# Optimization experiments

Measured on AMD Instinct MI355X. Metric: run time of the kernel, lower is better.

## Reference

```python
import jax, jax.numpy as jnp
import numpy as np

B, S, C = 128, 512, 128


def setup_inputs() -> dict:
    key = jax.random.key(0)
    k1, k2, k3, k4, k5 = jax.random.split(key, 5)
    emissions = jax.random.normal(k1, (B, S, C), dtype=jnp.float32)
    tags = jax.random.randint(k2, (B, S), 0, C, dtype=jnp.int64)
    mask = jnp.ones((B, S), dtype=bool)  # mask[:,0] must be True
    transitions = jax.random.normal(k3, (C, C), dtype=jnp.float32)
    start_transitions = jax.random.normal(k4, (C,), dtype=jnp.float32)
    end_transitions = jax.random.normal(k5, (C,), dtype=jnp.float32)
    return {"emissions": emissions, "tags": tags, "mask": mask,
            "transitions": transitions, "start_transitions": start_transitions,
            "end_transitions": end_transitions}


def _gold_score(emissions, tags, mask, transitions, start_t, end_t):
    # score of the gold tag path, fully vectorized over time
    b = jnp.arange(emissions.shape[0])
    score = start_t[tags[:, 0]] + emissions[b, 0, tags[:, 0]]            # [B]
    emit_t = jnp.take_along_axis(emissions, tags[..., None], axis=2)[..., 0]  # [B,S]
    trans_t = transitions[tags[:, :-1], tags[:, 1:]]                     # [B,S-1]
    score = score + jnp.sum((emit_t[:, 1:] + trans_t) * mask[:, 1:].astype(emissions.dtype), axis=1)
    last_idx = jnp.sum(mask.astype(jnp.int32), axis=1) - 1               # [B]
    last_tags = jnp.take_along_axis(tags, last_idx[:, None], axis=1)[:, 0]
    return score + end_t[last_tags]


def _partition(emissions, mask, transitions, start_t, end_t):
    # forward algorithm: sequential logsumexp recurrence via lax.scan
    alpha0 = start_t[None, :] + emissions[:, 0]                          # [B,C]

    def step(alpha, inp):
        emit_t, mask_t = inp                                             # [B,C], [B]
        score = alpha[:, :, None] + transitions[None] + emit_t[:, None, :]  # [B,C,C]
        new_alpha = jax.nn.logsumexp(score, axis=1)                      # [B,C]
        alpha = jnp.where(mask_t[:, None], new_alpha, alpha)
        return alpha, None

    xs = (jnp.moveaxis(emissions[:, 1:], 1, 0), mask[:, 1:].T)           # [S-1,B,C], [S-1,B]
    alpha, _ = jax.lax.scan(step, alpha0, xs)
    return jax.nn.logsumexp(alpha + end_t[None, :], axis=1)              # [B]


def reference(emissions, tags, mask, transitions, start_transitions, end_transitions):
    gold = _gold_score(emissions, tags, mask, transitions, start_transitions, end_transitions)
    part = _partition(emissions, mask, transitions, start_transitions, end_transitions)
    return -(gold - part).mean()
```

## Files before the change

kernel.cpp:

```cpp
#include <hip/hip_runtime.h>

#define BB 128
#define SS 512
#define CC 128

__device__ __forceinline__ void barrier_lgkm() {
    asm volatile("s_waitcnt lgkmcnt(0)" ::: "memory");
    __builtin_amdgcn_s_barrier();
}

__device__ __forceinline__ float lanebcast(float v, int i) {
    return __int_as_float(__builtin_amdgcn_readlane(__float_as_int(v), i));
}

__global__ __launch_bounds__(256, 1)
void crf_half_kernel(const float* __restrict__ emissions,
                     const int*   __restrict__ tags,
                     const float* __restrict__ transitions,
                     const float* __restrict__ start_t,
                     const float* __restrict__ end_t,
                     float* __restrict__ ws)
{
    const int  blk = blockIdx.x;
    const bool isF = (blk < BB);
    const int  b   = isF ? blk : (blk - BB);
    const int  tid = threadIdx.x;
    const int  wv  = tid >> 6;
    const int  q   = wv & 1;
    const int  h   = wv >> 1;
    const int  l   = tid & 63;
    const int  j   = h * 64 + l;
    const int  i   = q * 64 + l;

    float*  gold = ws;
    float*  xf   = ws + BB;
    float*  xb   = xf + BB * CC;
    double* Mf   = (double*)(xb + BB * CC);
    double* Mb   = Mf + BB;

    __shared__ float slot[2][2][CC];
    __shared__ float redg[4];

    const float* em_b = emissions + (size_t)b * SS * CC;

    float Ereg[64];
    {
        const float* Tb = transitions + (isF ? ((size_t)(q * 64) * CC + j)
                                             : ((size_t)j * CC + q * 64));
        const int us = isF ? CC : 1;
        #pragma unroll
        for (int t2 = 0; t2 < 64; ++t2) Ereg[t2] = __expf(Tb[(size_t)t2 * us]);
        #pragma unroll
        for (int t2 = 0; t2 < 64; ++t2) asm volatile("" : "+v"(Ereg[t2]));
    }

    float p = isF ? __expf(start_t[i] + em_b[i])
                  : __expf(end_t[i] + em_b[(size_t)(SS - 1) * CC + i]);
    double M = 0.0;

    const ptrdiff_t em_stride = isF ? (ptrdiff_t)CC : -(ptrdiff_t)CC;
    const float* em_base = em_b + j + (isF ? 3 * CC : 508 * CC);
    float ld0 = em_base[-2 * em_stride];
    float ld1 = em_base[-1 * em_stride];
    float ld2 = em_base[0];

#define SUBSTEP(T_, PAR, IS_BRIDGE) do {                                      \
        float a0=0.f, a1=0.f, a2=0.f, a3=0.f;                                 \
        _Pragma("unroll")                                                     \
        for (int uu = 0; uu < 16; ++uu) {                                     \
            a0 = fmaf(lanebcast(p, 4*uu+0), Ereg[4*uu+0], a0);                \
            a1 = fmaf(lanebcast(p, 4*uu+1), Ereg[4*uu+1], a1);                \
            a2 = fmaf(lanebcast(p, 4*uu+2), Ereg[4*uu+2], a2);                \
            a3 = fmaf(lanebcast(p, 4*uu+3), Ereg[4*uu+3], a3);                \
        }                                                                     \
        float part = (a0 + a1) + (a2 + a3);                                   \
        float ev = (IS_BRIDGE) ? 1.0f : __expf(ld0);                          \
        ld0 = ld1; ld1 = ld2;                                                 \
        ld2 = em_base[(ptrdiff_t)(T_) * em_stride];                           \
        slot[PAR][q][j] = part * ev;                        \
        barrier_lgkm();                                                       \
        float pn = slot[PAR][0][i] + slot[PAR][1][i];         \
        if (!(IS_BRIDGE) && ((T_) & 3) == 1) {                                \
            float r = slot[PAR][0][0] + slot[PAR][1][0];                      \
            float lr = __logf(r);                   \
            M += (double)lr;                                                  \
            pn *= __expf(-lr);                                                \
        }                                                                     \
        p = pn;                                                               \
    } while (0)

    #pragma unroll 1
    for (int t = 1; t < 255; t += 2) {
        SUBSTEP(t,     1, false);
        SUBSTEP(t + 1, 0, false);
    }
    SUBSTEP(255, 1, false);
    if (isF) SUBSTEP(256, 0, true);
#undef SUBSTEP

    if (h == 0) (isF ? xf : xb)[(size_t)b * CC + i] = p;
    if (tid == 0) { if (isF) Mf[b] = M; else Mb[b] = M; }

    if (!isF) {
        const int* tg = tags + b * SS;
        float g = 0.f;
        #pragma unroll
        for (int qq = 0; qq < 2; ++qq) {
            int t  = tid + qq * 256;
            int ct = tg[t];
            if (t == 0) g += start_t[ct] + em_b[ct] + end_t[tg[SS - 1]];
            else        g += em_b[(size_t)t * CC + ct] +
                             transitions[tg[t - 1] * CC + ct];
        }
        #pragma unroll
        for (int off = 32; off; off >>= 1) g += __shfl_down(g, off);
        if (l == 0) redg[wv] = g;
        __syncthreads();
        if (tid == 0) gold[b] = redg[0] + redg[1] + redg[2] + redg[3];
    }
}

__global__ __launch_bounds__(1024)
void crf_final_kernel(const float* __restrict__ ws, float* __restrict__ out)
{
    const float*  gold = ws;
    const float*  xf   = ws + BB;
    const float*  xb   = xf + BB * CC;
    const double* Mf   = (const double*)(xb + BB * CC);
    const double* Mb   = Mf + BB;

    const int tid = threadIdx.x;
    const int b   = tid >> 3;
    const int g   = tid & 7;

    const float* xa = xf + (size_t)b * CC + g * 16;
    const float* xc = xb + (size_t)b * CC + g * 16;
    float z = 0.f;
    #pragma unroll
    for (int k = 0; k < 16; ++k) z = fmaf(xa[k], xc[k], z);
    z += __shfl_down(z, 4);
    z += __shfl_down(z, 2);
    z += __shfl_down(z, 1);

    __shared__ float d_s[BB];
    __shared__ float red[2];
    if (g == 0) {
        double part = Mf[b] + Mb[b] + (double)__logf(z);
        d_s[b] = gold[b] - (float)part;
    }
    __syncthreads();

    float v = (tid < BB) ? d_s[tid] : 0.f;
    #pragma unroll
    for (int off = 32; off; off >>= 1) v += __shfl_down(v, off);
    if (tid == 0 || tid == 64) red[tid >> 6] = v;
    __syncthreads();
    if (tid == 0) out[0] = -(red[0] + red[1]) / (float)BB;
}

extern "C" void kernel_launch(void* const* d_in, const int* in_sizes, int n_in,
                              void* d_out, int out_size, void* d_ws, size_t ws_size,
                              hipStream_t stream) {
    const float* emissions   = (const float*)d_in[0];
    const int*   tags        = (const int*)d_in[1];
    const float* transitions = (const float*)d_in[3];
    const float* start_t     = (const float*)d_in[4];
    const float* end_t       = (const float*)d_in[5];
    float* out = (float*)d_out;
    float* ws  = (float*)d_ws;

    crf_half_kernel<<<2 * BB, 256, 0, stream>>>(emissions, tags, transitions,
                                                start_t, end_t, ws);
    crf_final_kernel<<<1, 1024, 0, stream>>>(ws, out);
}
```

Measured before the change: 175.1 us.

## Use two waves per block with own/other transition halves and one LDS exchange

Each block now runs two wavefronts instead of four. Each wave holds both its own and the other wave's 64-row slice of exp(transitions) in registers. The own-half dot product uses lane broadcasts of the wave's p, and the other half reads the partner wave's previous p from LDS as float4 vectors. This removes the partial-sum combine step and the second LDS read per timestep, and renormalisation now uses the previous step's value so the log-scaling is applied before the single barrier. The cost is 128 transition registers per lane and twice the FMA work per wave, which lengthens the serial critical path per step.

```diff
diff --git a/kernel.cpp b/kernel.cpp
--- a/kernel.cpp
+++ b/kernel.cpp
@@ -13,7 +13,7 @@
     return __int_as_float(__builtin_amdgcn_readlane(__float_as_int(v), i));
 }
 
-__global__ __launch_bounds__(256, 1)
+__global__ __launch_bounds__(128, 1)
 void crf_half_kernel(const float* __restrict__ emissions,
                      const int*   __restrict__ tags,
                      const float* __restrict__ transitions,
@@ -25,12 +25,10 @@
     const bool isF = (blk < BB);
     const int  b   = isF ? blk : (blk - BB);
     const int  tid = threadIdx.x;
-    const int  wv  = tid >> 6;
-    const int  q   = wv & 1;
-    const int  h   = wv >> 1;
+    const int  h   = tid >> 6;
     const int  l   = tid & 63;
     const int  j   = h * 64 + l;
-    const int  i   = q * 64 + l;
+    const int  ob  = (1 - h) * 64;
 
     float*  gold = ws;
     float*  xf   = ws + BB;
@@ -38,25 +36,35 @@
     double* Mf   = (double*)(xb + BB * CC);
     double* Mb   = Mf + BB;
 
-    __shared__ float slot[2][2][CC];
-    __shared__ float redg[4];
+    __shared__ __align__(16) float slot[2][CC];
+    __shared__ float redg[2];
 
     const float* em_b = emissions + (size_t)b * SS * CC;
 
-    float Ereg[64];
+    float Eown[64], Eoth[64];
     {
-        const float* Tb = transitions + (isF ? ((size_t)(q * 64) * CC + j)
-                                             : ((size_t)j * CC + q * 64));
-        const int us = isF ? CC : 1;
-        #pragma unroll
-        for (int t2 = 0; t2 < 64; ++t2) Ereg[t2] = __expf(Tb[(size_t)t2 * us]);
-        #pragma unroll
-        for (int t2 = 0; t2 < 64; ++t2) asm volatile("" : "+v"(Ereg[t2]));
-    }
-
-    float p = isF ? __expf(start_t[i] + em_b[i])
-                  : __expf(end_t[i] + em_b[(size_t)(SS - 1) * CC + i]);
+        const float *To, *Tt; int st;
+        if (isF) { To = transitions + (size_t)(h * 64) * CC + j;
+                   Tt = transitions + (size_t)ob * CC + j;       st = CC; }
+        else     { To = transitions + (size_t)j * CC + h * 64;
+                   Tt = transitions + (size_t)j * CC + ob;       st = 1;  }
+        #pragma unroll
+        for (int u = 0; u < 64; ++u) {
+            Eown[u] = __expf(To[(size_t)u * st]);
+            Eoth[u] = __expf(Tt[(size_t)u * st]);
+        }
+        #pragma unroll
+        for (int u = 0; u < 64; ++u) {
+            asm volatile("" : "+v"(Eown[u]));
+            asm volatile("" : "+v"(Eoth[u]));
+        }
+    }
+
+    float p = isF ? __expf(start_t[j] + em_b[j])
+                  : __expf(end_t[j] + em_b[(size_t)(SS - 1) * CC + j]);
     double M = 0.0;
+
+    slot[0][j] = p;
 
     const ptrdiff_t em_stride = isF ? (ptrdiff_t)CC : -(ptrdiff_t)CC;
     const float* em_base = em_b + j + (isF ? 3 * CC : 508 * CC);
@@ -64,49 +72,74 @@
     float ld1 = em_base[-1 * em_stride];
     float ld2 = em_base[0];
 
-#define SUBSTEP(T_, PAR, IS_BRIDGE) do {                                      \
+    barrier_lgkm();
+
+#define C4(K) do {                                                            \
+        a0 = fmaf(c##K.x, Eoth[4*K+0], a0);                                   \
+        a1 = fmaf(c##K.y, Eoth[4*K+1], a1);                                   \
+        a2 = fmaf(c##K.z, Eoth[4*K+2], a2);                                   \
+        a3 = fmaf(c##K.w, Eoth[4*K+3], a3);                                   \
+    } while (0)
+
+#define SUBSTEP(T_, PW, PP, RN, BRIDGE) do {                                  \
+           \
+        const float4* op = (const float4*)&slot[PP][ob];                      \
+        float4 c0=op[0],  c1=op[1],  c2=op[2],  c3=op[3];                     \
+        float4 c4=op[4],  c5=op[5],  c6=op[6],  c7=op[7];                     \
+        float4 c8=op[8],  c9=op[9],  c10=op[10],c11=op[11];                   \
+        float4 c12=op[12],c13=op[13],c14=op[14],c15=op[15];                   \
+        float rpv = (RN) ? slot[PP][0] : 1.0f;     \
         float a0=0.f, a1=0.f, a2=0.f, a3=0.f;                                 \
+                           \
         _Pragma("unroll")                                                     \
-        for (int uu = 0; uu < 16; ++uu) {                                     \
-            a0 = fmaf(lanebcast(p, 4*uu+0), Ereg[4*uu+0], a0);                \
-            a1 = fmaf(lanebcast(p, 4*uu+1), Ereg[4*uu+1], a1);                \
-            a2 = fmaf(lanebcast(p, 4*uu+2), Ereg[4*uu+2], a2);                \
-            a3 = fmaf(lanebcast(p, 4*uu+3), Ereg[4*uu+3], a3);                \
+        for (int u = 0; u < 16; ++u) {                                        \
+            a0 = fmaf(lanebcast(p, 4*u+0), Eown[4*u+0], a0);                  \
+            a1 = fmaf(lanebcast(p, 4*u+1), Eown[4*u+1], a1);                  \
+            a2 = fmaf(lanebcast(p, 4*u+2), Eown[4*u+2], a2);                  \
+            a3 = fmaf(lanebcast(p, 4*u+3), Eown[4*u+3], a3);                  \
         }                                                                     \
-        float part = (a0 + a1) + (a2 + a3);                                   \
-        float ev = (IS_BRIDGE) ? 1.0f : __expf(ld0);                          \
+                \
+        C4(0);  C4(1);  C4(2);  C4(3);  C4(4);  C4(5);  C4(6);  C4(7);        \
+        C4(8);  C4(9);  C4(10); C4(11); C4(12); C4(13); C4(14); C4(15);       \
+        float ev = (BRIDGE) ? 1.0f : __expf(ld0);                             \
         ld0 = ld1; ld1 = ld2;                                                 \
         ld2 = em_base[(ptrdiff_t)(T_) * em_stride];                           \
-        slot[PAR][q][j] = part * ev;                        \
-        barrier_lgkm();                                                       \
-        float pn = slot[PAR][0][i] + slot[PAR][1][i];         \
-        if (!(IS_BRIDGE) && ((T_) & 3) == 1) {                                \
-            float r = slot[PAR][0][0] + slot[PAR][1][0];                      \
-            float lr = __logf(r);                   \
+        if (RN) {                                                             \
+            float lr = __logf(rpv);                      \
             M += (double)lr;                                                  \
-            pn *= __expf(-lr);                                                \
+            ev *= __expf(-lr);                    \
         }                                                                     \
-        p = pn;                                                               \
+        float out = ((a0 + a1) + (a2 + a3)) * ev;                             \
+        if (!(BRIDGE)) {                                                      \
+            slot[PW][j] = out;                                                \
+            barrier_lgkm();                                                   \
+        }                                                                     \
+        p = out;                                                              \
     } while (0)
 
     #pragma unroll 1
     for (int t = 1; t < 255; t += 2) {
-        SUBSTEP(t,     1, false);
-        SUBSTEP(t + 1, 0, false);
-    }
-    SUBSTEP(255, 1, false);
-    if (isF) SUBSTEP(256, 0, true);
+        SUBSTEP(t,     1, 0, false, false);
+        SUBSTEP(t + 1, 0, 1, ((t & 3) == 1), false);
+    }
+    SUBSTEP(255, 1, 0, false, false);
+    if (isF) {
+        SUBSTEP(256, 0, 1, false, true);
+        xf[(size_t)b * CC + j] = p;
+        if (tid == 0) Mf[b] = M;
+    } else {
+        xb[(size_t)b * CC + j] = p;
+        if (tid == 0) Mb[b] = M;
+    }
 #undef SUBSTEP
-
-    if (h == 0) (isF ? xf : xb)[(size_t)b * CC + i] = p;
-    if (tid == 0) { if (isF) Mf[b] = M; else Mb[b] = M; }
+#undef C4
 
     if (!isF) {
         const int* tg = tags + b * SS;
         float g = 0.f;
         #pragma unroll
-        for (int qq = 0; qq < 2; ++qq) {
-            int t  = tid + qq * 256;
+        for (int qq = 0; qq < 4; ++qq) {
+            int t  = tid + qq * 128;
             int ct = tg[t];
             if (t == 0) g += start_t[ct] + em_b[ct] + end_t[tg[SS - 1]];
             else        g += em_b[(size_t)t * CC + ct] +
@@ -114,9 +147,9 @@
         }
         #pragma unroll
         for (int off = 32; off; off >>= 1) g += __shfl_down(g, off);
-        if (l == 0) redg[wv] = g;
+        if (l == 0) redg[h] = g;
         __syncthreads();
-        if (tid == 0) gold[b] = redg[0] + redg[1] + redg[2] + redg[3];
+        if (tid == 0) gold[b] = redg[0] + redg[1];
     }
 }
 
@@ -169,7 +202,7 @@
     float* out = (float*)d_out;
     float* ws  = (float*)d_ws;
 
-    crf_half_kernel<<<2 * BB, 256, 0, stream>>>(emissions, tags, transitions,
+    crf_half_kernel<<<2 * BB, 128, 0, stream>>>(emissions, tags, transitions,
                                                 start_t, end_t, ws);
     crf_final_kernel<<<1, 1024, 0, stream>>>(ws, out);
 }
```

Measured after the change: 227.3 us. 29.8% more time.

## Run bridge substep uniformly in both halves and split final reduction into two kernels

Applied to the files above, without the earlier changes.

The bridge substep now runs in both forward and backward blocks, with the backward blocks discarding its result. This removes the divergent branch and keeps the barriers uniform across the grid. The single 1024-thread final kernel is replaced by a per-batch combine kernel with 128 blocks and a small reduce kernel. This spreads the dot products across CUs but adds an extra kernel launch and a round trip through global memory.

```diff
diff --git a/kernel.cpp b/kernel.cpp
--- a/kernel.cpp
+++ b/kernel.cpp
@@ -86,6 +86,7 @@
             M += (double)lr;                                                  \
             pn *= __expf(-lr);                                                \
         }                                                                     \
+        if (IS_BRIDGE) pn = isF ? pn : p;    \
         p = pn;                                                               \
     } while (0)
 
@@ -95,7 +96,7 @@
         SUBSTEP(t + 1, 0, false);
     }
     SUBSTEP(255, 1, false);
-    if (isF) SUBSTEP(256, 0, true);
+    SUBSTEP(256, 0, true);
 #undef SUBSTEP
 
     if (h == 0) (isF ? xf : xb)[(size_t)b * CC + i] = p;
@@ -120,8 +121,8 @@
     }
 }
 
-__global__ __launch_bounds__(1024)
-void crf_final_kernel(const float* __restrict__ ws, float* __restrict__ out)
+__global__ __launch_bounds__(64)
+void crf_combine_kernel(const float* __restrict__ ws, float* __restrict__ d)
 {
     const float*  gold = ws;
     const float*  xf   = ws + BB;
@@ -129,31 +130,29 @@
     const double* Mf   = (const double*)(xb + BB * CC);
     const double* Mb   = Mf + BB;
 
+    const int b = blockIdx.x;
+    const int l = threadIdx.x;
+
+    const float* xa = xf + (size_t)b * CC;
+    const float* xc = xb + (size_t)b * CC;
+    float z = xa[l] * xc[l] + xa[64 + l] * xc[64 + l];
+    #pragma unroll
+    for (int off = 32; off; off >>= 1) z += __shfl_down(z, off);
+    if (l == 0) {
+        double part = Mf[b] + Mb[b] + (double)__logf(z);
+        d[b] = gold[b] - (float)part;
+    }
+}
+
+__global__ __launch_bounds__(128)
+void crf_reduce_kernel(const float* __restrict__ d, float* __restrict__ out)
+{
     const int tid = threadIdx.x;
-    const int b   = tid >> 3;
-    const int g   = tid & 7;
-
-    const float* xa = xf + (size_t)b * CC + g * 16;
-    const float* xc = xb + (size_t)b * CC + g * 16;
-    float z = 0.f;
-    #pragma unroll
-    for (int k = 0; k < 16; ++k) z = fmaf(xa[k], xc[k], z);
-    z += __shfl_down(z, 4);
-    z += __shfl_down(z, 2);
-    z += __shfl_down(z, 1);
-
-    __shared__ float d_s[BB];
-    __shared__ float red[2];
-    if (g == 0) {
-        double part = Mf[b] + Mb[b] + (double)__logf(z);
-        d_s[b] = gold[b] - (float)part;
-    }
-    __syncthreads();
-
-    float v = (tid < BB) ? d_s[tid] : 0.f;
+    float v = d[tid];
     #pragma unroll
     for (int off = 32; off; off >>= 1) v += __shfl_down(v, off);
-    if (tid == 0 || tid == 64) red[tid >> 6] = v;
+    __shared__ float red[2];
+    if ((tid & 63) == 0) red[tid >> 6] = v;
     __syncthreads();
     if (tid == 0) out[0] = -(red[0] + red[1]) / (float)BB;
 }
@@ -169,7 +168,10 @@
     float* out = (float*)d_out;
     float* ws  = (float*)d_ws;
 
+    float* dbuf = (float*)((double*)(ws + BB + 2 * BB * CC) + 2 * BB);
+
     crf_half_kernel<<<2 * BB, 256, 0, stream>>>(emissions, tags, transitions,
                                                 start_t, end_t, ws);
-    crf_final_kernel<<<1, 1024, 0, stream>>>(ws, out);
+    crf_combine_kernel<<<BB, 64, 0, stream>>>(ws, dbuf);
+    crf_reduce_kernel<<<1, 128, 0, stream>>>(dbuf, out);
 }
```

New measurement: 184.5 us. +5.4%, slower.
